# Kernel tuning notes

Measured on AMD Instinct MI355X. Metric: run time of the kernel, lower is better.

The kernel has to match this reference:

```python
import jax, jax.numpy as jnp
import numpy as np

B, S, D = 8, 1024, 512


def setup_inputs() -> dict:
    key = jax.random.key(0)
    k1, k2, k3, k4, k5, k6, k7 = jax.random.split(key, 7)
    inp = jax.random.normal(k1, (B, S, D), dtype=jnp.float32)
    aspect = jax.random.normal(k2, (B, S, D), dtype=jnp.float32)
    # lengths in [S//2, S], with max exactly S (the module requires max(len)==S)
    inp_len = jax.random.randint(k3, (B,), S // 2, S + 1).astype(jnp.float32)
    inp_len = inp_len.at[0].set(float(S))
    lim = float(np.sqrt(6.0 / (D + D)))  # xavier_uniform bound
    w1 = jax.random.uniform(k4, (D, D), jnp.float32, -lim, lim)
    b1 = jax.random.uniform(k5, (D,), jnp.float32, -lim, lim)
    w2 = jax.random.uniform(k6, (D, D), jnp.float32, -lim, lim)
    b2 = jax.random.uniform(k7, (D,), jnp.float32, -lim, lim)
    return {"inp": inp, "inp_len": inp_len, "aspect": aspect,
            "w1": w1, "b1": b1, "w2": w2, "b2": b2}


def reference(inp, inp_len, aspect, w1, b1, w2, b2):
    # inp, aspect: [B,S,D]; inp_len: [B] float lengths with max == S
    Bv, Sv, Dv = inp.shape
    scale = jnp.sqrt(inp_len)[:, None, None]                      # [B,1,1]
    att = jnp.einsum('bsd,btd->bst', aspect, inp) / scale          # [B,S,S]
    # mask over the query (row) dimension, as in the original expand
    mask = (jnp.arange(Sv)[None, :] < inp_len.astype(jnp.int32)[:, None]).astype(inp.dtype)  # [B,S]
    exp = att * mask[:, :, None]
    att_n = exp / (jnp.sum(exp, axis=-1, keepdims=True) + 1e-4)    # linear (non-exp) normalize
    weighted = jnp.einsum('bst,btd->bsd', att_n, inp)              # [B,S,D]
    ffn_inp = weighted + (inp + aspect) * mask[:, :, None]
    # FFN: two square linears with relu, plus inner residual
    o1 = jax.nn.relu(jnp.einsum('bsd,ed->bse', ffn_inp, w1) + b1)
    o2 = jax.nn.relu(jnp.einsum('bsd,ed->bse', o1, w2) + b2)
    ffn_out = o2 + ffn_inp
    final = ffn_inp + ffn_out
    return final / jnp.linalg.norm(final, axis=2, keepdims=True)
```

## Files before the change

kernel.cpp:

```cpp
#include <hip/hip_runtime.h>

#define Bq 8
#define Sq 1024
#define Dq 512

typedef __attribute__((ext_vector_type(8))) short bf16x8;
typedef __attribute__((ext_vector_type(4))) float f32x4;

__device__ __forceinline__ unsigned short f2bf(float f) {
  unsigned int u = __float_as_uint(f);
  return (unsigned short)((u + 0x7fffu + ((u >> 16) & 1u)) >> 16);
}

__device__ __forceinline__ void load_lds16(const unsigned short* g, unsigned short* l) {
  __builtin_amdgcn_global_load_lds(
      (const __attribute__((address_space(1))) unsigned int*)g,
      (__attribute__((address_space(3))) unsigned int*)l, 16, 0, 0);
}

__global__ __launch_bounds__(256) void prep_all(
    const float* __restrict__ inp, const float* __restrict__ aspect,
    const float* __restrict__ w1, const float* __restrict__ w2,
    unsigned short* __restrict__ inpT, float* __restrict__ partial,
    unsigned short* __restrict__ asp_bf,
    unsigned short* __restrict__ w1b, unsigned short* __restrict__ w2b) {
  __shared__ unsigned short tile[32][33];
  __shared__ float csum[8][33];
  int idx = blockIdx.x;
  int tid = threadIdx.x;
  if (idx < 4096) {
    int b = idx & 7;
    int tt = (idx >> 3) & 31;
    int t0 = tt * 32, d0 = (idx >> 8) * 32;
    int tx = tid & 31, ty = tid >> 5;
    const float* src = inp + ((size_t)b * Sq + t0) * Dq + d0;
    float part = 0.f;
#pragma unroll
    for (int i = 0; i < 4; ++i) {
      float v = src[(size_t)(ty + i * 8) * Dq + tx];
      tile[ty + i * 8][tx] = f2bf(v);
      part += v;
    }
    csum[ty][tx] = part;
    __syncthreads();
    unsigned short* dst = inpT + (size_t)b * Dq * Sq;
#pragma unroll
    for (int i = 0; i < 4; ++i)
      dst[(size_t)(d0 + ty + i * 8) * Sq + t0 + tx] = tile[tx][ty + i * 8];
    if (ty == 0) {
      float s = 0.f;
#pragma unroll
      for (int i = 0; i < 8; ++i) s += csum[i][tx];
      partial[((size_t)b * 32 + tt) * Dq + d0 + tx] = s;
    }
  } else if (idx < 4608) {
    int blk = idx - 4096;
    const float* s = aspect + (size_t)blk * 8192 + tid * 4;
    unsigned short* d = asp_bf + (size_t)blk * 8192 + tid * 4;
#pragma unroll
    for (int j = 0; j < 8; ++j) {
      float4 v = *(const float4*)(s + j * 1024);
      ushort4 o; o.x = f2bf(v.x); o.y = f2bf(v.y); o.z = f2bf(v.z); o.w = f2bf(v.w);
      *(ushort4*)(d + j * 1024) = o;
    }
  } else {
    int blk = idx - 4608;
    const float* src = (blk < 256) ? w1 : w2;
    unsigned short* dst = (blk < 256) ? w1b : w2b;
    int i = ((blk & 255) * 256 + tid) * 4;
    float4 v = *(const float4*)(src + i);
    ushort4 o; o.x = f2bf(v.x); o.y = f2bf(v.y); o.z = f2bf(v.z); o.w = f2bf(v.w);
    *(ushort4*)(dst + i) = o;
  }
}

__global__ __launch_bounds__(256, 5) void gram_fac(
    const unsigned short* __restrict__ inpT, const float* __restrict__ partial,
    const float* __restrict__ aspect, const float* __restrict__ lenv,
    unsigned short* __restrict__ Gm, float* __restrict__ fac) {
  __shared__ unsigned short sA[2][32 * 64];
  __shared__ unsigned short sB[2][64 * 64];
  int idx = blockIdx.x;
  int tid = threadIdx.x;
  int lane = tid & 63, wave = tid >> 6;

  if (idx >= 1024) {
    float* cs = (float*)sA;
    int fblk = idx - 1024;
    int b = fblk >> 6;
    int s0 = (fblk & 63) * 16;
#pragma unroll
    for (int h = 0; h < 2; ++h) {
      int d = h * 256 + tid;
      float s = 0.f;
      const float* p = partial + (size_t)b * 32 * Dq + d;
#pragma unroll
      for (int t = 0; t < 32; ++t) s += p[t * Dq];
      cs[d] = s;
    }
    __syncthreads();
    int g = lane >> 4, lr = lane & 15;
    int row = s0 + wave * 4 + g;
    const float* a = aspect + ((size_t)b * Sq + row) * Dq + lr * 32;
    float sum = 0.f;
#pragma unroll
    for (int j = 0; j < 8; ++j) {
      float4 v = *(const float4*)(a + j * 4);
      const float* c = cs + lr * 32 + j * 4;
      sum += v.x * c[0] + v.y * c[1] + v.z * c[2] + v.w * c[3];
    }
#pragma unroll
    for (int off = 1; off < 16; off <<= 1) sum += __shfl_xor(sum, off, 64);
    if (lr == 0) {
      float len = lenv[b];
      float scale = sqrtf(len);
      float f = 0.f;
      if (row < (int)len) f = 1.f / (scale * (sum / scale + 1e-4f));
      fac[b * Sq + row] = f;
    }
    return;
  }

  const int K = 1024;
  int b = idx & 7;
  int tile = idx >> 3;
  int bm = tile & 15, bn = tile >> 4;
  const unsigned short* Ab = inpT + (size_t)b * Dq * Sq + (size_t)bm * 32 * K;
  const unsigned short* Bb = inpT + (size_t)b * Dq * Sq + (size_t)bn * 64 * K;
  int lr = lane & 15, lq = lane >> 4;
  int x7 = lr & 7;
  int l3 = lane >> 3, l7 = lane & 7;

  const unsigned short* gA = Ab + (size_t)(wave * 8 + l3) * K + (l7 ^ l3) * 8;
  const unsigned short* gB = Bb + (size_t)(wave * 16 + l3) * K + (l7 ^ l3) * 8;
  int dbaseA = (wave * 64 + lane) * 8;
  int dbaseB0 = (wave * 128 + lane) * 8;
  int dbaseB1 = (wave * 128 + 64 + lane) * 8;

  f32x4 acc[2] = {};

  auto issue = [&](int buf, int k0) {
    load_lds16(gA + k0, &sA[buf][dbaseA]);
    load_lds16(gB + k0, &sB[buf][dbaseB0]);
    load_lds16(gB + (size_t)8 * K + k0, &sB[buf][dbaseB1]);
  };

  int wm = (wave & 1) * 16, wn = (wave >> 1) * 32;
  issue(0, 0);
#pragma unroll
  for (int it = 0; it < 16; ++it) {
    int cur = it & 1;
    __syncthreads();
    if (it + 1 < 16) issue(cur ^ 1, (it + 1) << 6);
#pragma unroll
    for (int c = 0; c < 2; ++c) {
      int g = c * 4 + lq;
      bf16x8 a0 = *(const bf16x8*)&sA[cur][((wm + lr) * 8 + (g ^ x7)) * 8];
      bf16x8 b0 = *(const bf16x8*)&sB[cur][((wn + lr) * 8 + (g ^ x7)) * 8];
      bf16x8 b1 = *(const bf16x8*)&sB[cur][((wn + 16 + lr) * 8 + (g ^ x7)) * 8];
      acc[0] = __builtin_amdgcn_mfma_f32_16x16x32_bf16(a0, b0, acc[0], 0, 0, 0);
      acc[1] = __builtin_amdgcn_mfma_f32_16x16x32_bf16(a0, b1, acc[1], 0, 0, 0);
    }
  }

  unsigned short* Ob = Gm + (size_t)b * 512 * 512;
#pragma unroll
  for (int ni = 0; ni < 2; ++ni)
#pragma unroll
    for (int i = 0; i < 4; ++i) {
      int r = bm * 32 + wm + lq * 4 + i;
      int cc = bn * 64 + wn + ni * 16 + lr;
      Ob[(size_t)r * 512 + cc] = f2bf(acc[ni][i]);
    }
}

#define LP 520
#define MEGA_SMEM (32 * LP * 2 + 2 * 32768 + 512)

__global__ __launch_bounds__(512, 2) void mega_ffn(
    const unsigned short* __restrict__ aspb, const unsigned short* __restrict__ G,
    const unsigned short* __restrict__ w1b, const unsigned short* __restrict__ w2b,
    const float* __restrict__ b1, const float* __restrict__ b2,
    const float* __restrict__ inp, const float* __restrict__ aspect,
    const float* __restrict__ fac, const float* __restrict__ lenv,
    float* __restrict__ out) {
  extern __shared__ char smem[];
  unsigned short* ldsA = (unsigned short*)smem;
  unsigned short* wbuf = (unsigned short*)(smem + 32 * LP * 2);
  float* ssqW = (float*)(smem + 32 * LP * 2 + 2 * 32768);
  int tid = threadIdx.x;
  int lane = tid & 63, wave = tid >> 6;
  int mg = wave >> 2, ng = wave & 3;
  int lr = lane & 15, lq = lane >> 4;
  int b = blockIdx.x & 7;
  int r0 = b * 1024 + (blockIdx.x >> 3) * 32;
  int c0 = ng * 128;
  int arow = r0 + mg * 16 + lr;

  bf16x8 af[16];
  f32x4 acc[8];
  f32x4 ffnv[8];

  auto stage = [&](int buf, int kc, const unsigned short* Bsrc) {
#pragma unroll
    for (int i = 0; i < 4; ++i) {
      int n = i * 128 + wave * 16 + (lane >> 2);
      load_lds16(Bsrc + (size_t)n * 512 + kc * 32 + (lane & 3) * 8,
                 wbuf + buf * 16384 + (size_t)(i * 512 + wave * 64 + lane) * 8);
    }
  };

  auto gemmPhase = [&](const unsigned short* Bsrc) {
#pragma unroll
    for (int t = 0; t < 8; ++t) acc[t] = (f32x4){0.f, 0.f, 0.f, 0.f};
    stage(0, 0, Bsrc);
#pragma unroll
    for (int kc = 0; kc < 16; ++kc) {
      int cur = kc & 1;
      __syncthreads();
      if (kc < 15) stage(cur ^ 1, kc + 1, Bsrc);
      bf16x8 bfr[8];
#pragma unroll
      for (int t = 0; t < 8; ++t)
        bfr[t] = *(const bf16x8*)&wbuf[cur * 16384 + (size_t)((c0 + t * 16 + lr) * 4 + lq) * 8];
#pragma unroll
      for (int t = 0; t < 8; ++t)
        acc[t] = __builtin_amdgcn_mfma_f32_16x16x32_bf16(af[kc], bfr[t], acc[t], 0, 0, 0);
    }
  };

#pragma unroll
  for (int j = 0; j < 16; ++j)
    af[j] = *(const bf16x8*)(aspb + (size_t)arow * 512 + j * 32 + lq * 8);
  gemmPhase(G + (size_t)b * 512 * 512);
  int len = (int)lenv[b];
  float facv[4];
#pragma unroll
  for (int i = 0; i < 4; ++i) facv[i] = fac[r0 + mg * 16 + lq * 4 + i];
#pragma unroll
  for (int t = 0; t < 8; ++t) {
#pragma unroll
    for (int i = 0; i < 4; ++i) {
      int r = r0 + mg * 16 + lq * 4 + i;
      size_t idx = (size_t)r * 512 + c0 + t * 16 + lr;
      float add = ((r & 1023) < len) ? (inp[idx] + aspect[idx]) : 0.f;
      float v = acc[t][i] * facv[i] + add;
      ffnv[t][i] = v;
      ldsA[(mg * 16 + lq * 4 + i) * LP + c0 + t * 16 + lr] = f2bf(v);
    }
  }
  __syncthreads();

#pragma unroll
  for (int j = 0; j < 16; ++j)
    af[j] = *(const bf16x8*)&ldsA[(mg * 16 + lr) * LP + j * 32 + lq * 8];
  __syncthreads();
  gemmPhase(w1b);
  float biasv[8];
#pragma unroll
  for (int t = 0; t < 8; ++t) biasv[t] = b1[c0 + t * 16 + lr];
#pragma unroll
  for (int t = 0; t < 8; ++t)
#pragma unroll
    for (int i = 0; i < 4; ++i)
      ldsA[(mg * 16 + lq * 4 + i) * LP + c0 + t * 16 + lr] =
          f2bf(fmaxf(acc[t][i] + biasv[t], 0.f));
  __syncthreads();

#pragma unroll
  for (int j = 0; j < 16; ++j)
    af[j] = *(const bf16x8*)&ldsA[(mg * 16 + lr) * LP + j * 32 + lq * 8];
  __syncthreads();
  gemmPhase(w2b);
#pragma unroll
  for (int t = 0; t < 8; ++t) biasv[t] = b2[c0 + t * 16 + lr];
  float ssq[4] = {0.f, 0.f, 0.f, 0.f};
#pragma unroll
  for (int t = 0; t < 8; ++t)
#pragma unroll
    for (int i = 0; i < 4; ++i) {
      float v = 2.f * ffnv[t][i] + fmaxf(acc[t][i] + biasv[t], 0.f);
      ffnv[t][i] = v;
      ssq[i] += v * v;
    }
#pragma unroll
  for (int off = 1; off < 16; off <<= 1)
#pragma unroll
    for (int i = 0; i < 4; ++i) ssq[i] += __shfl_xor(ssq[i], off, 64);
  if (lr == 0)
#pragma unroll
    for (int i = 0; i < 4; ++i) ssqW[(mg * 4 + ng) * 16 + lq * 4 + i] = ssq[i];
  __syncthreads();
  float rn[4];
#pragma unroll
  for (int i = 0; i < 4; ++i) {
    float s = ssqW[(mg * 4 + 0) * 16 + lq * 4 + i] + ssqW[(mg * 4 + 1) * 16 + lq * 4 + i] +
              ssqW[(mg * 4 + 2) * 16 + lq * 4 + i] + ssqW[(mg * 4 + 3) * 16 + lq * 4 + i];
    rn[i] = 1.f / sqrtf(s);
  }
#pragma unroll
  for (int t = 0; t < 8; ++t)
#pragma unroll
    for (int i = 0; i < 4; ++i) {
      int r = r0 + mg * 16 + lq * 4 + i;
      out[(size_t)r * 512 + c0 + t * 16 + lr] = ffnv[t][i] * rn[i];
    }
}

extern "C" void kernel_launch(void* const* d_in, const int* in_sizes, int n_in,
                              void* d_out, int out_size, void* d_ws, size_t ws_size,
                              hipStream_t stream) {
  const float* inp = (const float*)d_in[0];
  const float* inp_len = (const float*)d_in[1];
  const float* aspect = (const float*)d_in[2];
  const float* w1 = (const float*)d_in[3];
  const float* b1 = (const float*)d_in[4];
  const float* w2 = (const float*)d_in[5];
  const float* b2 = (const float*)d_in[6];
  float* out = (float*)d_out;

  char* W = (char*)d_ws;
  const size_t MB = 1ull << 20;
  unsigned short* asp_bf = (unsigned short*)(W + 0);
  unsigned short* inpT   = (unsigned short*)(W + 8 * MB);
  unsigned short* Gm     = (unsigned short*)(W + 16 * MB);
  unsigned short* w1bf   = (unsigned short*)(W + 20 * MB);
  unsigned short* w2bf   = (unsigned short*)(W + 20 * MB + 512 * 1024);
  float*          partial= (float*)(W + 21 * MB);
  float*          fac    = (float*)(W + 22 * MB);

  prep_all<<<5120, 256, 0, stream>>>(inp, aspect, w1, w2,
                                     inpT, partial, asp_bf, w1bf, w2bf);

  gram_fac<<<1536, 256, 0, stream>>>(inpT, partial, aspect, inp_len, Gm, fac);

  hipFuncSetAttribute((const void*)mega_ffn,
                      hipFuncAttributeMaxDynamicSharedMemorySize, MEGA_SMEM);
  mega_ffn<<<256, 512, MEGA_SMEM, stream>>>(
      asp_bf, Gm, w1bf, w2bf, b1, b2, inp, aspect, fac, inp_len, out);
}
```

Measured before the change: 158.8 us.

## Halve FFN row tile to 16 and XOR-swizzle the activation LDS buffer

The fused FFN kernel now handles 16 rows per block instead of 32. Each of the 8 waves owns 64 output columns, and the grid doubles to 512 blocks. The padded LDS activation layout becomes an XOR-swizzled layout, and the row-norm scratch reuses the start of that buffer, which cuts shared memory per block. Launch bounds are raised to allow more resident blocks. The aim is more parallelism and occupancy across CUs, at the cost of each block streaming the full G, w1 and w2 matrices for half as many rows, which doubles weight traffic.

```diff
diff --git a/kernel.cpp b/kernel.cpp
--- a/kernel.cpp
+++ b/kernel.cpp
@@ -174,10 +174,9 @@
     }
 }
 
-#define LP 520
-#define MEGA_SMEM (32 * LP * 2 + 2 * 32768 + 512)
-
-__global__ __launch_bounds__(512, 2) void mega_ffn(
+#define MEGA_SMEM (16384 + 65536)
+
+__global__ __launch_bounds__(512, 4) void mega_ffn(
     const unsigned short* __restrict__ aspb, const unsigned short* __restrict__ G,
     const unsigned short* __restrict__ w1b, const unsigned short* __restrict__ w2b,
     const float* __restrict__ b1, const float* __restrict__ b2,
@@ -186,20 +185,18 @@
     float* __restrict__ out) {
   extern __shared__ char smem[];
   unsigned short* ldsA = (unsigned short*)smem;
-  unsigned short* wbuf = (unsigned short*)(smem + 32 * LP * 2);
-  float* ssqW = (float*)(smem + 32 * LP * 2 + 2 * 32768);
+  unsigned short* wbuf = (unsigned short*)(smem + 16384);
+  float* ssqW = (float*)smem;
   int tid = threadIdx.x;
   int lane = tid & 63, wave = tid >> 6;
-  int mg = wave >> 2, ng = wave & 3;
   int lr = lane & 15, lq = lane >> 4;
   int b = blockIdx.x & 7;
-  int r0 = b * 1024 + (blockIdx.x >> 3) * 32;
-  int c0 = ng * 128;
-  int arow = r0 + mg * 16 + lr;
+  int r0 = b * 1024 + (blockIdx.x >> 3) * 16;
+  int c0 = wave * 64;
 
   bf16x8 af[16];
-  f32x4 acc[8];
-  f32x4 ffnv[8];
+  f32x4 acc[4];
+  f32x4 ffnv[4];
 
   auto stage = [&](int buf, int kc, const unsigned short* Bsrc) {
 #pragma unroll
@@ -212,71 +209,76 @@
 
   auto gemmPhase = [&](const unsigned short* Bsrc) {
 #pragma unroll
-    for (int t = 0; t < 8; ++t) acc[t] = (f32x4){0.f, 0.f, 0.f, 0.f};
+    for (int t = 0; t < 4; ++t) acc[t] = (f32x4){0.f, 0.f, 0.f, 0.f};
     stage(0, 0, Bsrc);
 #pragma unroll
     for (int kc = 0; kc < 16; ++kc) {
       int cur = kc & 1;
       __syncthreads();
       if (kc < 15) stage(cur ^ 1, kc + 1, Bsrc);
-      bf16x8 bfr[8];
-#pragma unroll
-      for (int t = 0; t < 8; ++t)
+      bf16x8 bfr[4];
+#pragma unroll
+      for (int t = 0; t < 4; ++t)
         bfr[t] = *(const bf16x8*)&wbuf[cur * 16384 + (size_t)((c0 + t * 16 + lr) * 4 + lq) * 8];
 #pragma unroll
-      for (int t = 0; t < 8; ++t)
+      for (int t = 0; t < 4; ++t)
         acc[t] = __builtin_amdgcn_mfma_f32_16x16x32_bf16(af[kc], bfr[t], acc[t], 0, 0, 0);
     }
   };
 
+  auto ldsA_store = [&](int rl, int c, unsigned short v) {
+    int g = c >> 3;
+    ldsA[(rl * 64 + (g ^ (rl & 7))) * 8 + (c & 7)] = v;
+  };
+
+  const unsigned short* aspRow = aspb + (size_t)(r0 + lr) * 512;
 #pragma unroll
   for (int j = 0; j < 16; ++j)
-    af[j] = *(const bf16x8*)(aspb + (size_t)arow * 512 + j * 32 + lq * 8);
+    af[j] = *(const bf16x8*)(aspRow + j * 32 + lq * 8);
   gemmPhase(G + (size_t)b * 512 * 512);
   int len = (int)lenv[b];
   float facv[4];
 #pragma unroll
-  for (int i = 0; i < 4; ++i) facv[i] = fac[r0 + mg * 16 + lq * 4 + i];
-#pragma unroll
-  for (int t = 0; t < 8; ++t) {
-#pragma unroll
-    for (int i = 0; i < 4; ++i) {
-      int r = r0 + mg * 16 + lq * 4 + i;
+  for (int i = 0; i < 4; ++i) facv[i] = fac[r0 + lq * 4 + i];
+#pragma unroll
+  for (int t = 0; t < 4; ++t) {
+#pragma unroll
+    for (int i = 0; i < 4; ++i) {
+      int r = r0 + lq * 4 + i;
       size_t idx = (size_t)r * 512 + c0 + t * 16 + lr;
       float add = ((r & 1023) < len) ? (inp[idx] + aspect[idx]) : 0.f;
       float v = acc[t][i] * facv[i] + add;
       ffnv[t][i] = v;
-      ldsA[(mg * 16 + lq * 4 + i) * LP + c0 + t * 16 + lr] = f2bf(v);
+      ldsA_store(lq * 4 + i, c0 + t * 16 + lr, f2bf(v));
     }
   }
   __syncthreads();
 
 #pragma unroll
   for (int j = 0; j < 16; ++j)
-    af[j] = *(const bf16x8*)&ldsA[(mg * 16 + lr) * LP + j * 32 + lq * 8];
+    af[j] = *(const bf16x8*)&ldsA[(lr * 64 + ((j * 4 + lq) ^ (lr & 7))) * 8];
   __syncthreads();
   gemmPhase(w1b);
-  float biasv[8];
-#pragma unroll
-  for (int t = 0; t < 8; ++t) biasv[t] = b1[c0 + t * 16 + lr];
-#pragma unroll
-  for (int t = 0; t < 8; ++t)
+  float biasv[4];
+#pragma unroll
+  for (int t = 0; t < 4; ++t) biasv[t] = b1[c0 + t * 16 + lr];
+#pragma unroll
+  for (int t = 0; t < 4; ++t)
 #pragma unroll
     for (int i = 0; i < 4; ++i)
-      ldsA[(mg * 16 + lq * 4 + i) * LP + c0 + t * 16 + lr] =
-          f2bf(fmaxf(acc[t][i] + biasv[t], 0.f));
+      ldsA_store(lq * 4 + i, c0 + t * 16 + lr, f2bf(fmaxf(acc[t][i] + biasv[t], 0.f)));
   __syncthreads();
 
 #pragma unroll
   for (int j = 0; j < 16; ++j)
-    af[j] = *(const bf16x8*)&ldsA[(mg * 16 + lr) * LP + j * 32 + lq * 8];
+    af[j] = *(const bf16x8*)&ldsA[(lr * 64 + ((j * 4 + lq) ^ (lr & 7))) * 8];
   __syncthreads();
   gemmPhase(w2b);
 #pragma unroll
-  for (int t = 0; t < 8; ++t) biasv[t] = b2[c0 + t * 16 + lr];
+  for (int t = 0; t < 4; ++t) biasv[t] = b2[c0 + t * 16 + lr];
   float ssq[4] = {0.f, 0.f, 0.f, 0.f};
 #pragma unroll
-  for (int t = 0; t < 8; ++t)
+  for (int t = 0; t < 4; ++t)
 #pragma unroll
     for (int i = 0; i < 4; ++i) {
       float v = 2.f * ffnv[t][i] + fmaxf(acc[t][i] + biasv[t], 0.f);
@@ -289,20 +291,21 @@
     for (int i = 0; i < 4; ++i) ssq[i] += __shfl_xor(ssq[i], off, 64);
   if (lr == 0)
 #pragma unroll
-    for (int i = 0; i < 4; ++i) ssqW[(mg * 4 + ng) * 16 + lq * 4 + i] = ssq[i];
+    for (int i = 0; i < 4; ++i) ssqW[wave * 16 + lq * 4 + i] = ssq[i];
   __syncthreads();
   float rn[4];
 #pragma unroll
   for (int i = 0; i < 4; ++i) {
-    float s = ssqW[(mg * 4 + 0) * 16 + lq * 4 + i] + ssqW[(mg * 4 + 1) * 16 + lq * 4 + i] +
-              ssqW[(mg * 4 + 2) * 16 + lq * 4 + i] + ssqW[(mg * 4 + 3) * 16 + lq * 4 + i];
+    float s = 0.f;
+#pragma unroll
+    for (int g = 0; g < 8; ++g) s += ssqW[g * 16 + lq * 4 + i];
     rn[i] = 1.f / sqrtf(s);
   }
 #pragma unroll
-  for (int t = 0; t < 8; ++t)
-#pragma unroll
-    for (int i = 0; i < 4; ++i) {
-      int r = r0 + mg * 16 + lq * 4 + i;
+  for (int t = 0; t < 4; ++t)
+#pragma unroll
+    for (int i = 0; i < 4; ++i) {
+      int r = r0 + lq * 4 + i;
       out[(size_t)r * 512 + c0 + t * 16 + lr] = ffnv[t][i] * rn[i];
     }
 }
@@ -336,6 +339,6 @@
 
   hipFuncSetAttribute((const void*)mega_ffn,
                       hipFuncAttributeMaxDynamicSharedMemorySize, MEGA_SMEM);
-  mega_ffn<<<256, 512, MEGA_SMEM, stream>>>(
+  mega_ffn<<<512, 512, MEGA_SMEM, stream>>>(
       asp_bf, Gm, w1bf, w2bf, b1, b2, inp, aspect, fac, inp_len, out);
 }
```

Result: slower. 185.4 us (+16.7%).
